# Optimization experiments

Hardware: AMD Instinct MI355X
Metric: run time of the kernel (lower is better)

Reference implementation:

```python
import jax, jax.numpy as jnp
import numpy as np

D = 42            # node hidden dim
ED = 10           # edge feature dim
B = 512           # graphs per batch
NU, EU = 16384, 32768   # solute nodes/edges (32 nodes per graph)
NV, EV = 20480, 40960   # solvent nodes/edges (40 nodes per graph)
STEPS = 6


def setup_inputs() -> dict:
    key = jax.random.key(0)
    ks = iter(jax.random.split(key, 48))
    nrm = lambda shape, s: jax.random.normal(next(ks), shape, dtype=jnp.float32) * s
    inp = {}
    inp["su_x"] = nrm((NU, D), 1.0)
    inp["su_e"] = nrm((EU, ED), 1.0)
    inp["su_src"] = jax.random.randint(next(ks), (EU,), 0, NU, dtype=jnp.int32)
    inp["su_dst"] = jax.random.randint(next(ks), (EU,), 0, NU, dtype=jnp.int32)
    inp["sv_x"] = nrm((NV, D), 1.0)
    inp["sv_e"] = nrm((EV, ED), 1.0)
    inp["sv_src"] = jax.random.randint(next(ks), (EV,), 0, NV, dtype=jnp.int32)
    inp["sv_dst"] = jax.random.randint(next(ks), (EV,), 0, NV, dtype=jnp.int32)
    for p in ("su", "sv"):
        inp[p + "_lin0_w"] = nrm((D, D), D ** -0.5)
        inp[p + "_lin0_b"] = jnp.zeros((D,), jnp.float32)
        inp[p + "_msg_w"] = nrm((D, D), D ** -0.5)
        inp[p + "_msg_b"] = jnp.zeros((D,), jnp.float32)
        inp[p + "_en1_w"] = nrm((ED, ED), ED ** -0.5)
        inp[p + "_en1_b"] = jnp.zeros((ED,), jnp.float32)
        inp[p + "_en2_w"] = nrm((ED, D * D), 0.02)  # small scale keeps 6-step recursion stable
        inp[p + "_en2_b"] = jnp.zeros((D * D,), jnp.float32)
        inp[p + "_conv_b"] = jnp.zeros((D,), jnp.float32)
    inp["fc1_w"] = nrm((4 * D, 256), (4 * D) ** -0.5)
    inp["fc1_b"] = jnp.zeros((256,), jnp.float32)
    inp["fc2_w"] = nrm((256, 128), 256 ** -0.5)
    inp["fc2_b"] = jnp.zeros((128,), jnp.float32)
    inp["fc3_w"] = nrm((128, 1), 128 ** -0.5)
    inp["fc3_b"] = jnp.zeros((1,), jnp.float32)
    return inp


def _gather(x, efeat, src, dst, lw, lb, mw, mb, e1w, e1b, e2w, e2b, cb, n_nodes):
    """GatherModel: lin0 + 6 x (NNConv(sum, residual=identity, bias) -> relu -> message_layer -> relu) + skip."""
    init = x
    out = jax.nn.relu(x @ lw + lb)
    # Edge network depends only on static edge features -> compute per-edge 42x42 once.
    We = (jax.nn.relu(efeat @ e1w + e1b) @ e2w + e2b).reshape(-1, D, D)  # [E, D, D]
    for _ in range(STEPS):
        msg = jnp.einsum('ei,eio->eo', out[src], We)                    # gather + per-edge matvec
        agg = jax.ops.segment_sum(msg, dst, num_segments=n_nodes)      # scatter-add
        m = jax.nn.relu(agg + out + cb)                                 # residual (identity) + bias, then relu
        out = jax.nn.relu(m @ mw + mb)
    return out + init


def reference(su_x, su_e, su_src, su_dst, sv_x, sv_e, sv_src, sv_dst,
              su_lin0_w, su_lin0_b, su_msg_w, su_msg_b, su_en1_w, su_en1_b, su_en2_w, su_en2_b, su_conv_b,
              sv_lin0_w, sv_lin0_b, sv_msg_w, sv_msg_b, sv_en1_w, sv_en1_b, sv_en2_w, sv_en2_b, sv_conv_b,
              fc1_w, fc1_b, fc2_w, fc2_b, fc3_w, fc3_b):
    su = _gather(su_x, su_e, su_src, su_dst, su_lin0_w, su_lin0_b, su_msg_w, su_msg_b,
                 su_en1_w, su_en1_b, su_en2_w, su_en2_b, su_conv_b, NU)
    sv = _gather(sv_x, sv_e, sv_src, sv_dst, sv_lin0_w, sv_lin0_b, sv_msg_w, sv_msg_b,
                 sv_en1_w, sv_en1_b, sv_en2_w, sv_en2_b, sv_conv_b, NV)
    # per-graph mean pooling (equal-sized graphs -> reshape)
    su_emb = su.reshape(B, NU // B, D).mean(axis=1)          # [B, D]
    sv_emb = sv.reshape(B, NV // B, D).mean(axis=1)
    su_fin = jnp.concatenate([su_emb, su_emb], axis=1)       # [B, 2D]
    sv_fin = jnp.concatenate([sv_emb, sv_emb], axis=1)
    su_g = su_fin.mean(axis=0, keepdims=True)                # [1, 2D] (code means over batch)
    sv_g = sv_fin.mean(axis=0, keepdims=True)
    comb = jnp.concatenate([su_g, sv_g], axis=1)             # [1, 4D]
    h = jax.nn.relu(comb @ fc1_w + fc1_b)                    # dropout is identity at inference
    h = jax.nn.relu(h @ fc2_w + fc2_b)
    pred = h @ fc3_w + fc3_b                                 # [1, 1]
    interaction = jnp.zeros((su.shape[0], sv.shape[0]), jnp.float32)
    return pred, interaction
```

## Files before the change

### kernel.cpp

```cpp
#include <hip/hip_runtime.h>

#define D   42
#define ED  10
#define NU  16384
#define EU  32768
#define NV  20480
#define EV  40960
#define NT  (NU + NV)
#define ET  (EU + EV)
#define GJ  462
#define GS  512
#define STEPS 6

typedef float floatx4 __attribute__((ext_vector_type(4)));

__global__ __launch_bounds__(256) void k_zero(floatx4* __restrict__ p, long n4,
                                              float* __restrict__ tail, int ntail) {
    long stride = (long)gridDim.x * 256;
    floatx4 z = (floatx4)(0.f);
    for (long i = blockIdx.x * 256L + threadIdx.x; i < n4; i += stride)
        __builtin_nontemporal_store(z, &p[i]);
    if (blockIdx.x == 0 && threadIdx.x < ntail)
        tail[threadIdx.x] = 0.f;
}

__global__ void k_prep(const float* __restrict__ su_w2, const float* __restrict__ su_b2,
                       const float* __restrict__ sv_w2, const float* __restrict__ sv_b2,
                       float* __restrict__ A, float* __restrict__ mean) {
    int gid = blockIdx.x * 256 + threadIdx.x;
    if (gid < 128) mean[gid] = 0.f;
    if (gid >= 2 * D * GS) return;
    int phase = gid / (D * GS);
    int r = gid - phase * D * GS;
    int i = r / GS, j = r - i * GS;
    const float* w2 = phase ? sv_w2 : su_w2;
    const float* b2 = phase ? sv_b2 : su_b2;
    float v = 0.f;
    if (j < GJ) {
        int k = j / D, o = j - k * D;
        v = (k < ED) ? w2[k * (D * D) + i * D + o] : b2[i * D + o];
    }
    A[gid] = v;
}

__global__ void k_lin0(const float* __restrict__ su_x, const float* __restrict__ sv_x,
                       const float* __restrict__ su_w, const float* __restrict__ su_b,
                       const float* __restrict__ sv_w, const float* __restrict__ sv_b,
                       float* __restrict__ out) {
    int gid = blockIdx.x * 256 + threadIdx.x;
    if (gid >= NT * D) return;
    int n = gid / D, o = gid - n * D;
    const float *x, *w, *b; int nl;
    if (n < NU) { x = su_x; w = su_w; b = su_b; nl = n; }
    else        { x = sv_x; w = sv_w; b = sv_b; nl = n - NU; }
    float s = b[o];
    #pragma unroll
    for (int i = 0; i < D; i++) s += x[nl * D + i] * w[i * D + o];
    out[gid] = fmaxf(s, 0.f);
}

__global__ void k_edgeh(const float* __restrict__ su_e, const float* __restrict__ sv_e,
                        const float* __restrict__ su_w1, const float* __restrict__ su_b1,
                        const float* __restrict__ sv_w1, const float* __restrict__ sv_b1,
                        float* __restrict__ h) {
    __shared__ float w1s[2][ED * ED];
    __shared__ float b1s[2][ED];
    int tid = threadIdx.x;
    if (tid < ED * ED) { w1s[0][tid] = su_w1[tid]; w1s[1][tid] = sv_w1[tid]; }
    if (tid < ED)      { b1s[0][tid] = su_b1[tid]; b1s[1][tid] = sv_b1[tid]; }
    __syncthreads();
    int e = blockIdx.x * 256 + tid;
    if (e >= ET) return;
    int ph = (e >= EU);
    const float* ef = ph ? (sv_e + (size_t)(e - EU) * ED) : (su_e + (size_t)e * ED);
    float v[ED];
    #pragma unroll
    for (int j = 0; j < ED; j++) v[j] = ef[j];
    #pragma unroll
    for (int k = 0; k < ED; k++) {
        float s = b1s[ph][k];
        #pragma unroll
        for (int j = 0; j < ED; j++) s += v[j] * w1s[ph][j * ED + k];
        h[e * 12 + k] = fmaxf(s, 0.f);
    }
    h[e * 12 + 10] = 1.f;
    h[e * 12 + 11] = 0.f;
}

__global__ __launch_bounds__(512, 1) void k_g(const float* __restrict__ out,
                                              const float* __restrict__ A,
                                              float* __restrict__ g,
                                              float* __restrict__ agg) {
    __shared__ float As[D * GS];
    __shared__ float outT[D * 36];
    int tid = threadIdx.x;
    int n0 = blockIdx.x * 32;
    const float4* Ag = (const float4*)(A + (n0 >= NU ? D * GS : 0));
    float4* As4 = (float4*)As;
    for (int idx = tid; idx < D * GS / 4; idx += 512) As4[idx] = Ag[idx];
    for (int idx = tid; idx < 32 * D; idx += 512) {
        int nn = idx / D, i = idx - nn * D;
        outT[i * 36 + nn] = out[(size_t)(n0 + nn) * D + i];
    }
    for (int idx = tid; idx < 32 * D; idx += 512) agg[(size_t)n0 * D + idx] = 0.f;
    __syncthreads();

    int tj = tid & 127;
    int tn = tid >> 7;
    float4 acc[8];
    #pragma unroll
    for (int r = 0; r < 8; r++) acc[r] = make_float4(0.f, 0.f, 0.f, 0.f);
    const float4* outT4 = (const float4*)outT;

    for (int i = 0; i < D; i++) {
        float4 a  = As4[i * (GS / 4) + tj];
        float4 o0 = outT4[i * 9 + tn * 2];
        float4 o1 = outT4[i * 9 + tn * 2 + 1];
#define MAC(rr, ov) acc[rr].x += a.x * (ov); acc[rr].y += a.y * (ov); \
                    acc[rr].z += a.z * (ov); acc[rr].w += a.w * (ov);
        MAC(0, o0.x) MAC(1, o0.y) MAC(2, o0.z) MAC(3, o0.w)
        MAC(4, o1.x) MAC(5, o1.y) MAC(6, o1.z) MAC(7, o1.w)
#undef MAC
    }
    float4* g4 = (float4*)g;
    #pragma unroll
    for (int r = 0; r < 8; r++) {
        int n = n0 + tn * 8 + r;
        g4[(size_t)n * (GS / 4) + tj] = acc[r];
    }
}

__global__ void k_edge(const float* __restrict__ g, const float* __restrict__ h,
                       const int* __restrict__ su_src, const int* __restrict__ su_dst,
                       const int* __restrict__ sv_src, const int* __restrict__ sv_dst,
                       float* __restrict__ agg) {
    int gid = blockIdx.x * 256 + threadIdx.x;
    if (gid >= ET * D) return;
    int e = gid / D, o = gid - e * D;
    int src, dst;
    if (e < EU) { src = su_src[e];           dst = su_dst[e]; }
    else        { src = sv_src[e - EU] + NU; dst = sv_dst[e - EU] + NU; }
    const float* grow = g + (size_t)src * GS;
    const float* hrow = h + (size_t)e * 12;
    float s = 0.f;
    #pragma unroll
    for (int k = 0; k <= ED; k++) s += hrow[k] * grow[k * D + o];
    atomicAdd(&agg[(size_t)dst * D + o], s);
}

__global__ void k_update(const float* __restrict__ agg, float* __restrict__ out,
                         const float* __restrict__ su_mw, const float* __restrict__ su_mb,
                         const float* __restrict__ su_cb,
                         const float* __restrict__ sv_mw, const float* __restrict__ sv_mb,
                         const float* __restrict__ sv_cb) {
    __shared__ float mws[D * D];
    __shared__ float mloc[32 * D];
    int tid = threadIdx.x;
    int n0 = blockIdx.x * 32;
    int ph = (n0 >= NU);
    const float* mw = ph ? sv_mw : su_mw;
    const float* mb = ph ? sv_mb : su_mb;
    const float* cb = ph ? sv_cb : su_cb;
    for (int idx = tid; idx < D * D; idx += 256) mws[idx] = mw[idx];
    for (int idx = tid; idx < 32 * D; idx += 256) {
        float v = agg[(size_t)n0 * D + idx] + out[(size_t)n0 * D + idx] + cb[idx % D];
        mloc[idx] = fmaxf(v, 0.f);
    }
    __syncthreads();
    for (int idx = tid; idx < 32 * D; idx += 256) {
        int nn = idx / D, o = idx - nn * D;
        float s = mb[o];
        #pragma unroll
        for (int i = 0; i < D; i++) s += mloc[nn * D + i] * mws[i * D + o];
        out[(size_t)n0 * D + idx] = fmaxf(s, 0.f);
    }
}

__global__ void k_reduce(const float* __restrict__ out, const float* __restrict__ su_x,
                         const float* __restrict__ sv_x, float* __restrict__ mean) {
    __shared__ float sdata[6 * D];
    int tid = threadIdx.x;
    int bid = blockIdx.x;
    int n0, ph, nl0;
    const float* x;
    if (bid < NU / 128) { ph = 0; n0 = bid * 128;               nl0 = n0;      x = su_x; }
    else                { ph = 1; n0 = NU + (bid - NU/128)*128; nl0 = n0 - NU; x = sv_x; }
    if (tid < 6 * D) {
        int o = tid % D, r = tid / D;
        float acc = 0.f;
        for (int nn = r; nn < 128; nn += 6)
            acc += out[(size_t)(n0 + nn) * D + o] + x[(size_t)(nl0 + nn) * D + o];
        sdata[r * D + o] = acc;
    }
    __syncthreads();
    if (tid < D) {
        float tot = 0.f;
        #pragma unroll
        for (int r = 0; r < 6; r++) tot += sdata[r * D + tid];
        atomicAdd(&mean[ph * D + tid], tot);
    }
}

__global__ void k_mlp(const float* __restrict__ mean,
                      const float* __restrict__ fc1w, const float* __restrict__ fc1b,
                      const float* __restrict__ fc2w, const float* __restrict__ fc2b,
                      const float* __restrict__ fc3w, const float* __restrict__ fc3b,
                      float* __restrict__ outp) {
    __shared__ float c[4 * D];
    __shared__ float h1[256];
    __shared__ float h2[128];
    int t = threadIdx.x;
    if (t < 4 * D) {
        float v;
        if (t < 2 * D) v = mean[t < D ? t : t - D] * (1.f / NU);
        else { int q = t - 2 * D; v = mean[D + (q < D ? q : q - D)] * (1.f / NV); }
        c[t] = v;
    }
    __syncthreads();
    float s = fc1b[t];
    for (int j = 0; j < 4 * D; j++) s += c[j] * fc1w[j * 256 + t];
    h1[t] = fmaxf(s, 0.f);
    __syncthreads();
    if (t < 128) {
        float s2 = fc2b[t];
        for (int j = 0; j < 256; j++) s2 += h1[j] * fc2w[j * 128 + t];
        h2[t] = fmaxf(s2, 0.f);
    }
    __syncthreads();
    if (t == 0) {
        float s3 = fc3b[0];
        for (int j = 0; j < 128; j++) s3 += h2[j] * fc3w[j];
        outp[0] = s3;
    }
}

extern "C" void kernel_launch(void* const* d_in, const int* in_sizes, int n_in,
                              void* d_out, int out_size, void* d_ws, size_t ws_size,
                              hipStream_t stream) {
    const float* su_x     = (const float*)d_in[0];
    const float* su_e     = (const float*)d_in[1];
    const int*   su_src   = (const int*)d_in[2];
    const int*   su_dst   = (const int*)d_in[3];
    const float* sv_x     = (const float*)d_in[4];
    const float* sv_e     = (const float*)d_in[5];
    const int*   sv_src   = (const int*)d_in[6];
    const int*   sv_dst   = (const int*)d_in[7];
    const float* su_lin0w = (const float*)d_in[8];
    const float* su_lin0b = (const float*)d_in[9];
    const float* su_msgw  = (const float*)d_in[10];
    const float* su_msgb  = (const float*)d_in[11];
    const float* su_en1w  = (const float*)d_in[12];
    const float* su_en1b  = (const float*)d_in[13];
    const float* su_en2w  = (const float*)d_in[14];
    const float* su_en2b  = (const float*)d_in[15];
    const float* su_convb = (const float*)d_in[16];
    const float* sv_lin0w = (const float*)d_in[17];
    const float* sv_lin0b = (const float*)d_in[18];
    const float* sv_msgw  = (const float*)d_in[19];
    const float* sv_msgb  = (const float*)d_in[20];
    const float* sv_en1w  = (const float*)d_in[21];
    const float* sv_en1b  = (const float*)d_in[22];
    const float* sv_en2w  = (const float*)d_in[23];
    const float* sv_en2b  = (const float*)d_in[24];
    const float* sv_convb = (const float*)d_in[25];
    const float* fc1w     = (const float*)d_in[26];
    const float* fc1b     = (const float*)d_in[27];
    const float* fc2w     = (const float*)d_in[28];
    const float* fc2b     = (const float*)d_in[29];
    const float* fc3w     = (const float*)d_in[30];
    const float* fc3b     = (const float*)d_in[31];

    float* ws   = (float*)d_ws;
    float* out  = ws;
    float* g    = out  + (size_t)NT * D;
    float* h    = g    + (size_t)NT * GS;
    float* agg  = h    + (size_t)ET * 12;
    float* A    = agg  + (size_t)NT * D;
    float* mean = A    + (size_t)2 * D * GS;

    {
        long n4 = ((long)out_size * 4) / 16;
        int ntail = (int)(out_size - n4 * 4);
        float* tailp = (float*)d_out + n4 * 4;
        k_zero<<<2048, 256, 0, stream>>>((floatx4*)d_out, n4, tailp, ntail);
    }

    k_prep<<<(2 * D * GS + 255) / 256, 256, 0, stream>>>(su_en2w, su_en2b, sv_en2w, sv_en2b, A, mean);
    k_lin0<<<(NT * D + 255) / 256, 256, 0, stream>>>(su_x, sv_x, su_lin0w, su_lin0b, sv_lin0w, sv_lin0b, out);
    k_edgeh<<<(ET + 255) / 256, 256, 0, stream>>>(su_e, sv_e, su_en1w, su_en1b, sv_en1w, sv_en1b, h);

    for (int s = 0; s < STEPS; s++) {
        k_g<<<NT / 32, 512, 0, stream>>>(out, A, g, agg);
        k_edge<<<(ET * D + 255) / 256, 256, 0, stream>>>(g, h, su_src, su_dst, sv_src, sv_dst, agg);
        k_update<<<NT / 32, 256, 0, stream>>>(agg, out, su_msgw, su_msgb, su_convb,
                                              sv_msgw, sv_msgb, sv_convb);
    }

    k_reduce<<<NU / 128 + NV / 128, 256, 0, stream>>>(out, su_x, sv_x, mean);
    k_mlp<<<1, 256, 0, stream>>>(mean, fc1w, fc1b, fc2w, fc2b, fc3w, fc3b, (float*)d_out);
}
```

Before: 865.2 us.

## Build CSR edge ordering and fuse per-node g computation with edge messages

Builds CSR-style out-edge and in-edge orderings once per call using count, scan and place kernels. The per-node edge-network product g now stays in LDS and is consumed in the same kernel to emit per-edge messages, so the large g buffer no longer round-trips through global memory. Aggregation becomes a deterministic pull over in-edges instead of float atomics, which also removes the agg zeroing. The cost is extra setup kernels, including a single-block scan, and a per-edge msg buffer in global memory. The inner g padding also shrinks from 512 to 464.

```diff
diff --git a/kernel.cpp b/kernel.cpp
--- a/kernel.cpp
+++ b/kernel.cpp
@@ -9,7 +9,7 @@
 #define NT  (NU + NV)
 #define ET  (EU + EV)
 #define GJ  462
-#define GS  512
+#define GP  464
 #define STEPS 6
 
 typedef float floatx4 __attribute__((ext_vector_type(4)));
@@ -29,10 +29,10 @@
                        float* __restrict__ A, float* __restrict__ mean) {
     int gid = blockIdx.x * 256 + threadIdx.x;
     if (gid < 128) mean[gid] = 0.f;
-    if (gid >= 2 * D * GS) return;
-    int phase = gid / (D * GS);
-    int r = gid - phase * D * GS;
-    int i = r / GS, j = r - i * GS;
+    if (gid >= 2 * D * GP) return;
+    int phase = gid / (D * GP);
+    int r = gid - phase * D * GP;
+    int i = r / GP, j = r - i * GP;
     const float* w2 = phase ? sv_w2 : su_w2;
     const float* b2 = phase ? sv_b2 : su_b2;
     float v = 0.f;
@@ -59,10 +59,73 @@
     out[gid] = fmaxf(s, 0.f);
 }
 
+__global__ void k_zcnt(int* __restrict__ p, int n) {
+    int gid = blockIdx.x * 256 + threadIdx.x;
+    if (gid < n) p[gid] = 0;
+}
+
+__global__ void k_count(const int* __restrict__ su_src, const int* __restrict__ su_dst,
+                        const int* __restrict__ sv_src, const int* __restrict__ sv_dst,
+                        int* __restrict__ outDeg, int* __restrict__ inDeg) {
+    int e = blockIdx.x * 256 + threadIdx.x;
+    if (e >= ET) return;
+    int src, dst;
+    if (e < EU) { src = su_src[e];           dst = su_dst[e]; }
+    else        { src = sv_src[e - EU] + NU; dst = sv_dst[e - EU] + NU; }
+    atomicAdd(&outDeg[src], 1);
+    atomicAdd(&inDeg[dst], 1);
+}
+
+__global__ __launch_bounds__(1024) void k_scan(const int* __restrict__ degO, int* __restrict__ offO,
+                                               const int* __restrict__ degI, int* __restrict__ offI) {
+    __shared__ int part[1024];
+    int t = threadIdx.x;
+    for (int a = 0; a < 2; a++) {
+        const int* deg = a ? degI : degO;
+        int* off = a ? offI : offO;
+        int loc[36];
+        int base = t * 36;
+        int s = 0;
+        #pragma unroll
+        for (int j = 0; j < 36; j++) { loc[j] = s; s += deg[base + j]; }
+        part[t] = s;
+        __syncthreads();
+        for (int d = 1; d < 1024; d <<= 1) {
+            int v = (t >= d) ? part[t - d] : 0;
+            __syncthreads();
+            part[t] += v;
+            __syncthreads();
+        }
+        int excl = part[t] - s;
+        #pragma unroll
+        for (int j = 0; j < 36; j++) off[base + j] = excl + loc[j];
+        if (t == 1023) off[NT] = excl + s;
+        __syncthreads();
+    }
+}
+
+__global__ void k_place(const int* __restrict__ su_src, const int* __restrict__ su_dst,
+                        const int* __restrict__ sv_src, const int* __restrict__ sv_dst,
+                        const int* __restrict__ offO, int* __restrict__ cntO,
+                        const int* __restrict__ offI, int* __restrict__ cntI,
+                        int* __restrict__ inList, int* __restrict__ srcSorted,
+                        int* __restrict__ pOf) {
+    int e = blockIdx.x * 256 + threadIdx.x;
+    if (e >= ET) return;
+    int src, dst;
+    if (e < EU) { src = su_src[e];           dst = su_dst[e]; }
+    else        { src = sv_src[e - EU] + NU; dst = sv_dst[e - EU] + NU; }
+    int p = offO[src] + atomicAdd(&cntO[src], 1);
+    int q = offI[dst] + atomicAdd(&cntI[dst], 1);
+    inList[q] = p;
+    srcSorted[p] = src;
+    pOf[e] = p;
+}
+
 __global__ void k_edgeh(const float* __restrict__ su_e, const float* __restrict__ sv_e,
                         const float* __restrict__ su_w1, const float* __restrict__ su_b1,
                         const float* __restrict__ sv_w1, const float* __restrict__ sv_b1,
-                        float* __restrict__ h) {
+                        const int* __restrict__ pOf, float* __restrict__ hs) {
     __shared__ float w1s[2][ED * ED];
     __shared__ float b1s[2][ED];
     int tid = threadIdx.x;
@@ -76,103 +139,102 @@
     float v[ED];
     #pragma unroll
     for (int j = 0; j < ED; j++) v[j] = ef[j];
+    size_t p = (size_t)pOf[e] * 12;
     #pragma unroll
     for (int k = 0; k < ED; k++) {
         float s = b1s[ph][k];
         #pragma unroll
         for (int j = 0; j < ED; j++) s += v[j] * w1s[ph][j * ED + k];
-        h[e * 12 + k] = fmaxf(s, 0.f);
-    }
-    h[e * 12 + 10] = 1.f;
-    h[e * 12 + 11] = 0.f;
-}
-
-__global__ __launch_bounds__(512, 1) void k_g(const float* __restrict__ out,
-                                              const float* __restrict__ A,
-                                              float* __restrict__ g,
-                                              float* __restrict__ agg) {
-    __shared__ float As[D * GS];
-    __shared__ float outT[D * 36];
+        hs[p + k] = fmaxf(s, 0.f);
+    }
+    hs[p + 10] = 1.f;
+    hs[p + 11] = 0.f;
+}
+
+__global__ __launch_bounds__(512, 1) void k_gmsg(const float* __restrict__ out,
+                                                 const float* __restrict__ A,
+                                                 const int* __restrict__ offO,
+                                                 const int* __restrict__ srcSorted,
+                                                 const float* __restrict__ hs,
+                                                 float* __restrict__ msg) {
+    __shared__ float A_lds[D * GP];
+    __shared__ float g_lds[32 * GP];
+    __shared__ float out_lds[32 * 44];
     int tid = threadIdx.x;
     int n0 = blockIdx.x * 32;
-    const float4* Ag = (const float4*)(A + (n0 >= NU ? D * GS : 0));
-    float4* As4 = (float4*)As;
-    for (int idx = tid; idx < D * GS / 4; idx += 512) As4[idx] = Ag[idx];
+    const floatx4* Ag = (const floatx4*)(A + (n0 >= NU ? D * GP : 0));
+    floatx4* Al4 = (floatx4*)A_lds;
+    for (int idx = tid; idx < D * GP / 4; idx += 512) Al4[idx] = Ag[idx];
     for (int idx = tid; idx < 32 * D; idx += 512) {
         int nn = idx / D, i = idx - nn * D;
-        outT[i * 36 + nn] = out[(size_t)(n0 + nn) * D + i];
-    }
-    for (int idx = tid; idx < 32 * D; idx += 512) agg[(size_t)n0 * D + idx] = 0.f;
+        out_lds[nn * 44 + i] = out[(size_t)(n0 + nn) * D + i];
+    }
     __syncthreads();
 
     int tj = tid & 127;
     int tn = tid >> 7;
-    float4 acc[8];
-    #pragma unroll
-    for (int r = 0; r < 8; r++) acc[r] = make_float4(0.f, 0.f, 0.f, 0.f);
-    const float4* outT4 = (const float4*)outT;
-
-    for (int i = 0; i < D; i++) {
-        float4 a  = As4[i * (GS / 4) + tj];
-        float4 o0 = outT4[i * 9 + tn * 2];
-        float4 o1 = outT4[i * 9 + tn * 2 + 1];
-#define MAC(rr, ov) acc[rr].x += a.x * (ov); acc[rr].y += a.y * (ov); \
-                    acc[rr].z += a.z * (ov); acc[rr].w += a.w * (ov);
-        MAC(0, o0.x) MAC(1, o0.y) MAC(2, o0.z) MAC(3, o0.w)
-        MAC(4, o1.x) MAC(5, o1.y) MAC(6, o1.z) MAC(7, o1.w)
-#undef MAC
-    }
-    float4* g4 = (float4*)g;
-    #pragma unroll
-    for (int r = 0; r < 8; r++) {
-        int n = n0 + tn * 8 + r;
-        g4[(size_t)n * (GS / 4) + tj] = acc[r];
-    }
-}
-
-__global__ void k_edge(const float* __restrict__ g, const float* __restrict__ h,
-                       const int* __restrict__ su_src, const int* __restrict__ su_dst,
-                       const int* __restrict__ sv_src, const int* __restrict__ sv_dst,
-                       float* __restrict__ agg) {
-    int gid = blockIdx.x * 256 + threadIdx.x;
-    if (gid >= ET * D) return;
-    int e = gid / D, o = gid - e * D;
-    int src, dst;
-    if (e < EU) { src = su_src[e];           dst = su_dst[e]; }
-    else        { src = sv_src[e - EU] + NU; dst = sv_dst[e - EU] + NU; }
-    const float* grow = g + (size_t)src * GS;
-    const float* hrow = h + (size_t)e * 12;
-    float s = 0.f;
-    #pragma unroll
-    for (int k = 0; k <= ED; k++) s += hrow[k] * grow[k * D + o];
-    atomicAdd(&agg[(size_t)dst * D + o], s);
-}
-
-__global__ void k_update(const float* __restrict__ agg, float* __restrict__ out,
-                         const float* __restrict__ su_mw, const float* __restrict__ su_mb,
-                         const float* __restrict__ su_cb,
-                         const float* __restrict__ sv_mw, const float* __restrict__ sv_mb,
-                         const float* __restrict__ sv_cb) {
-    __shared__ float mws[D * D];
-    __shared__ float mloc[32 * D];
+    if (tj < 116) {
+        floatx4 acc[8];
+        #pragma unroll
+        for (int r = 0; r < 8; r++) acc[r] = (floatx4)(0.f);
+        for (int i = 0; i < D; i++) {
+            floatx4 a = Al4[i * 116 + tj];
+            #pragma unroll
+            for (int r = 0; r < 8; r++) acc[r] += a * out_lds[(tn * 8 + r) * 44 + i];
+        }
+        floatx4* gl4 = (floatx4*)g_lds;
+        #pragma unroll
+        for (int r = 0; r < 8; r++) gl4[(tn * 8 + r) * 116 + tj] = acc[r];
+    }
+    __syncthreads();
+
+    int p0 = offO[n0], p1 = offO[n0 + 32];
+    int nwork = (p1 - p0) * D;
+    for (int idx = tid; idx < nwork; idx += 512) {
+        int pr = idx / D, o = idx - pr * D;
+        int p = p0 + pr;
+        int local = srcSorted[p] - n0;
+        const float* hrow = hs + (size_t)p * 12;
+        const float* grow = g_lds + local * GP;
+        float s = 0.f;
+        #pragma unroll
+        for (int k = 0; k <= ED; k++) s += hrow[k] * grow[k * D + o];
+        msg[(size_t)p * D + o] = s;
+    }
+}
+
+__global__ __launch_bounds__(256) void k_upd(const int* __restrict__ offI,
+                                             const int* __restrict__ inList,
+                                             const float* __restrict__ msg,
+                                             float* __restrict__ out,
+                                             const float* __restrict__ su_mw, const float* __restrict__ su_mb,
+                                             const float* __restrict__ su_cb,
+                                             const float* __restrict__ sv_mw, const float* __restrict__ sv_mb,
+                                             const float* __restrict__ sv_cb) {
+    __shared__ float mw_lds[D * D];
+    __shared__ float m_lds[32 * 44];
     int tid = threadIdx.x;
     int n0 = blockIdx.x * 32;
     int ph = (n0 >= NU);
     const float* mw = ph ? sv_mw : su_mw;
     const float* mb = ph ? sv_mb : su_mb;
     const float* cb = ph ? sv_cb : su_cb;
-    for (int idx = tid; idx < D * D; idx += 256) mws[idx] = mw[idx];
+    for (int idx = tid; idx < D * D; idx += 256) mw_lds[idx] = mw[idx];
     for (int idx = tid; idx < 32 * D; idx += 256) {
-        float v = agg[(size_t)n0 * D + idx] + out[(size_t)n0 * D + idx] + cb[idx % D];
-        mloc[idx] = fmaxf(v, 0.f);
+        int nn = idx / D, o = idx - nn * D;
+        int n = n0 + nn;
+        int q0 = offI[n], q1 = offI[n + 1];
+        float s = out[(size_t)n * D + o] + cb[o];
+        for (int q = q0; q < q1; q++) s += msg[(size_t)inList[q] * D + o];
+        m_lds[nn * 44 + o] = fmaxf(s, 0.f);
     }
     __syncthreads();
     for (int idx = tid; idx < 32 * D; idx += 256) {
         int nn = idx / D, o = idx - nn * D;
         float s = mb[o];
         #pragma unroll
-        for (int i = 0; i < D; i++) s += mloc[nn * D + i] * mws[i * D + o];
-        out[(size_t)n0 * D + idx] = fmaxf(s, 0.f);
+        for (int i = 0; i < D; i++) s += m_lds[nn * 44 + i] * mw_lds[i * D + o];
+        out[(size_t)(n0 + nn) * D + o] = fmaxf(s, 0.f);
     }
 }
 
@@ -183,8 +245,8 @@
     int bid = blockIdx.x;
     int n0, ph, nl0;
     const float* x;
-    if (bid < NU / 128) { ph = 0; n0 = bid * 128;               nl0 = n0;      x = su_x; }
-    else                { ph = 1; n0 = NU + (bid - NU/128)*128; nl0 = n0 - NU; x = sv_x; }
+    if (bid < NU / 128) { ph = 0; n0 = bid * 128;                 nl0 = n0;      x = su_x; }
+    else                { ph = 1; n0 = NU + (bid - NU/128) * 128; nl0 = n0 - NU; x = sv_x; }
     if (tid < 6 * D) {
         int o = tid % D, r = tid / D;
         float acc = 0.f;
@@ -272,11 +334,20 @@
 
     float* ws   = (float*)d_ws;
     float* out  = ws;
-    float* g    = out  + (size_t)NT * D;
-    float* h    = g    + (size_t)NT * GS;
-    float* agg  = h    + (size_t)ET * 12;
-    float* A    = agg  + (size_t)NT * D;
-    float* mean = A    + (size_t)2 * D * GS;
+    float* msg  = out  + (size_t)NT * D;
+    float* hs   = msg  + (size_t)ET * D;
+    float* A    = hs   + (size_t)ET * 12;
+    float* mean = A    + (size_t)2 * D * GP;
+    int* ib     = (int*)(mean + 128);
+    int* outDeg = ib;
+    int* inDeg  = outDeg + NT;
+    int* outCnt = inDeg  + NT;
+    int* inCnt  = outCnt + NT;
+    int* outOff = inCnt  + NT;
+    int* inOff  = outOff + (NT + 1);
+    int* inList = inOff  + (NT + 1);
+    int* srcS   = inList + ET;
+    int* pOf    = srcS   + ET;
 
     {
         long n4 = ((long)out_size * 4) / 16;
@@ -285,15 +356,20 @@
         k_zero<<<2048, 256, 0, stream>>>((floatx4*)d_out, n4, tailp, ntail);
     }
 
-    k_prep<<<(2 * D * GS + 255) / 256, 256, 0, stream>>>(su_en2w, su_en2b, sv_en2w, sv_en2b, A, mean);
+    k_prep<<<(2 * D * GP + 255) / 256, 256, 0, stream>>>(su_en2w, su_en2b, sv_en2w, sv_en2b, A, mean);
     k_lin0<<<(NT * D + 255) / 256, 256, 0, stream>>>(su_x, sv_x, su_lin0w, su_lin0b, sv_lin0w, sv_lin0b, out);
-    k_edgeh<<<(ET + 255) / 256, 256, 0, stream>>>(su_e, sv_e, su_en1w, su_en1b, sv_en1w, sv_en1b, h);
+
+    k_zcnt<<<(4 * NT + 255) / 256, 256, 0, stream>>>(outDeg, 4 * NT);
+    k_count<<<(ET + 255) / 256, 256, 0, stream>>>(su_src, su_dst, sv_src, sv_dst, outDeg, inDeg);
+    k_scan<<<1, 1024, 0, stream>>>(outDeg, outOff, inDeg, inOff);
+    k_place<<<(ET + 255) / 256, 256, 0, stream>>>(su_src, su_dst, sv_src, sv_dst,
+                                                  outOff, outCnt, inOff, inCnt, inList, srcS, pOf);
+    k_edgeh<<<(ET + 255) / 256, 256, 0, stream>>>(su_e, sv_e, su_en1w, su_en1b, sv_en1w, sv_en1b, pOf, hs);
 
     for (int s = 0; s < STEPS; s++) {
-        k_g<<<NT / 32, 512, 0, stream>>>(out, A, g, agg);
-        k_edge<<<(ET * D + 255) / 256, 256, 0, stream>>>(g, h, su_src, su_dst, sv_src, sv_dst, agg);
-        k_update<<<NT / 32, 256, 0, stream>>>(agg, out, su_msgw, su_msgb, su_convb,
-                                              sv_msgw, sv_msgb, sv_convb);
+        k_gmsg<<<NT / 32, 512, 0, stream>>>(out, A, outOff, srcS, hs, msg);
+        k_upd<<<NT / 32, 256, 0, stream>>>(inOff, inList, msg, out,
+                                           su_msgw, su_msgb, su_convb, sv_msgw, sv_msgb, sv_convb);
     }
 
     k_reduce<<<NU / 128 + NV / 128, 256, 0, stream>>>(out, su_x, sv_x, mean);
```

Measured after the change: 875.1 us. About the same (+1.1%).
